# Optimization experiments

Hardware: AMD Instinct MI355X
Metric: run time of the kernel (lower is better)

## Reference

```python
import jax, jax.numpy as jnp
import numpy as np
from jax import lax

PATCH = 9
DILATION = 1
EPS = 1e-6


def _l2norm(x):
    # L2-normalize over channel dim (dim=1), eps added to sum of squares before sqrt
    norm = jnp.sqrt(jnp.sum(x * x, axis=1, keepdims=True) + EPS)
    return x / norm


def setup_inputs() -> dict:
    key = jax.random.key(0)
    k1, k2 = jax.random.split(key)
    feature1 = jax.random.normal(k1, (4, 64, 64, 64), dtype=jnp.float32)
    feature2 = jax.random.normal(k2, (4, 64, 64, 64), dtype=jnp.float32)
    return {"feature1": feature1, "feature2": feature2}


def _correlation(f1, f2, patch, dilation):
    # SpatialCorrelationSampler with ks=1, stride=1, pad=0:
    # corr[b, pi, pj, y, x] = sum_c f1[b,c,y,x] * f2[b,c,y+dy,x+dx]
    # dy = (pi - patch//2)*dilation, dx = (pj - patch//2)*dilation; OOB = 0.
    b, c, h, w = f1.shape
    half = (patch // 2) * dilation
    f2p = jnp.pad(f2, ((0, 0), (0, 0), (half, half), (half, half)))
    d = jnp.arange(patch, dtype=jnp.int32) * dilation  # offsets into padded map
    offs = jnp.stack(jnp.meshgrid(d, d, indexing="ij"), axis=-1).reshape(-1, 2)  # [P^2, 2]

    def one_disp(off):
        f2s = lax.dynamic_slice(f2p, (0, 0, off[0], off[1]), (b, c, h, w))
        return jnp.sum(f1 * f2s, axis=1)  # [b, h, w]

    corr = lax.map(one_disp, offs)  # [P^2, b, h, w] (sequential -> low peak memory)
    return jnp.transpose(corr, (1, 0, 2, 3))  # [b, P^2, h, w]


def reference(feature1, feature2):
    f1 = _l2norm(feature1)
    f2 = _l2norm(feature2)
    b, c, h, w = f1.shape
    corr = _correlation(f1, f2, PATCH, DILATION)  # [b, P^2, h, w]
    corr = corr.reshape(b, PATCH * PATCH, h * w)
    return jax.nn.relu(corr)
```

## Files before the change

kernel.cpp:

```cpp
#include <hip/hip_runtime.h>

#define BB 4
#define CC 64
#define C2 32
#define HH 64
#define WW 64
#define PATCH 9
#define HALF 4
#define P2 81
#define HW (HH * WW)
#define IMG (CC * HW)

typedef _Float16 v2h __attribute__((ext_vector_type(2)));


__global__ __launch_bounds__(128) void prep_kernel(const float* __restrict__ f1,
                                                   const float* __restrict__ f2,
                                                   unsigned* __restrict__ nf) {
    int gid = blockIdx.x * 128 + threadIdx.x;
    int img = gid >> 14;
    int b   = (gid >> 12) & 3;
    int p   = gid & 4095;
    const float* src = (img ? f2 : f1) + b * IMG + p;
    float v[CC];
    float ss = 0.f;
#pragma unroll
    for (int c = 0; c < CC; ++c) { float t = src[c * HW]; v[c] = t; ss += t * t; }
    float inv = rsqrtf(ss + 1e-6f);
    unsigned* dst = nf + img * 524288 + b * 131072 + p;
#pragma unroll
    for (int c2 = 0; c2 < C2; ++c2) {
        v2h h = { (_Float16)(v[2 * c2] * inv), (_Float16)(v[2 * c2 + 1] * inv) };
        dst[c2 * 4096] = __builtin_bit_cast(unsigned, h);
    }
}

__global__ __launch_bounds__(576) void corr_kernel(const unsigned* __restrict__ nf,
                                                   float* __restrict__ out) {
    __shared__ unsigned sB[PATCH * C2 * 72];
    __shared__ unsigned sA[C2 * 64];

    const int tid = threadIdx.x;
    const int x  = tid & 63;
    const int dy = tid >> 6;
    const int b  = blockIdx.x >> 6;
    const int y  = blockIdx.x & 63;

    const unsigned* nf1b = nf + b * 131072;
    const unsigned* nf2b = nf + 524288 + b * 131072;

    if (tid < 512) {
        int c2 = tid >> 4, k = tid & 15;
        *(uint4*)&sA[c2 * 64 + k * 4] = *(const uint4*)&nf1b[c2 * 4096 + y * 64 + k * 4];
    }
#pragma unroll
    for (int it = 0; it < 8; ++it) {
        int item = tid + it * 576;
        int dyy = item >> 9;
        int rem = item & 511;
        int c2 = rem >> 4, k = rem & 15;
        int y2 = y + dyy - HALF;
        uint4 vv = {0u, 0u, 0u, 0u};
        if ((unsigned)y2 < HH)
            vv = *(const uint4*)&nf2b[c2 * 4096 + y2 * 64 + k * 4];
        *(uint4*)&sB[(dyy * C2 + c2) * 72 + 4 + k * 4] = vv;
    }
#pragma unroll
    for (int j = tid; j < 2304; j += 576) {
        int row = j >> 3, e = j & 7;
        sB[row * 72 + (e < 4 ? e : 64 + e)] = 0u;
    }
    __syncthreads();

    float acc[PATCH];
#pragma unroll
    for (int i = 0; i < PATCH; ++i) acc[i] = 0.f;

#pragma unroll
    for (int c2 = 0; c2 < C2; ++c2) {
        v2h a2 = __builtin_bit_cast(v2h, sA[c2 * 64 + x]);
        const unsigned* br = &sB[(dy * C2 + c2) * 72 + x];
#pragma unroll
        for (int dx = 0; dx < PATCH; ++dx)
            acc[dx] = __builtin_amdgcn_fdot2(a2, __builtin_bit_cast(v2h, br[dx]),
                                             acc[dx], false);
    }

    float* ob = out + b * P2 * HW + y * WW + x;
#pragma unroll
    for (int dx = 0; dx < PATCH; ++dx)
        ob[(dy * PATCH + dx) * HW] = fmaxf(acc[dx], 0.f);
}

extern "C" void kernel_launch(void* const* d_in, const int* in_sizes, int n_in,
                              void* d_out, int out_size, void* d_ws, size_t ws_size,
                              hipStream_t stream) {
    const float* f1 = (const float*)d_in[0];
    const float* f2 = (const float*)d_in[1];
    float* out = (float*)d_out;
    unsigned* nf = (unsigned*)d_ws;

    prep_kernel<<<256, 128, 0, stream>>>(f1, f2, nf);
    corr_kernel<<<BB * HH, 576, 0, stream>>>(nf, out);
}
```

Measured before the change: 70.76 us.

## Fuse L2 normalization into correlation kernel via post-scaling by inverse norms

Removes the separate prep kernel that normalized and packed features to fp16 in a workspace. The correlation kernel now reads raw fp32 features, packs them to fp16 in shared memory, computes inverse norms per pixel from the shared tiles, and scales the dot products by both norms before the ReLU. This eliminates one launch and a global-memory round trip. In exchange it reads twice the bytes per staged element, recomputes norms redundantly across blocks, and rounds unnormalized values to fp16.

New measurement: 70.34 us. Within noise of the previous version (-0.6%).

```diff
diff --git a/kernel.cpp b/kernel.cpp
--- a/kernel.cpp
+++ b/kernel.cpp
@@ -8,37 +8,23 @@
 #define PATCH 9
 #define HALF 4
 #define P2 81
-#define HW (HH * WW)
+#define HW 4096
 #define IMG (CC * HW)
 
 typedef _Float16 v2h __attribute__((ext_vector_type(2)));
 
-
-__global__ __launch_bounds__(128) void prep_kernel(const float* __restrict__ f1,
-                                                   const float* __restrict__ f2,
-                                                   unsigned* __restrict__ nf) {
-    int gid = blockIdx.x * 128 + threadIdx.x;
-    int img = gid >> 14;
-    int b   = (gid >> 12) & 3;
-    int p   = gid & 4095;
-    const float* src = (img ? f2 : f1) + b * IMG + p;
-    float v[CC];
-    float ss = 0.f;
-#pragma unroll
-    for (int c = 0; c < CC; ++c) { float t = src[c * HW]; v[c] = t; ss += t * t; }
-    float inv = rsqrtf(ss + 1e-6f);
-    unsigned* dst = nf + img * 524288 + b * 131072 + p;
-#pragma unroll
-    for (int c2 = 0; c2 < C2; ++c2) {
-        v2h h = { (_Float16)(v[2 * c2] * inv), (_Float16)(v[2 * c2 + 1] * inv) };
-        dst[c2 * 4096] = __builtin_bit_cast(unsigned, h);
-    }
+static __device__ __forceinline__ unsigned pk(float a, float b) {
+    v2h h = {(_Float16)a, (_Float16)b};
+    return __builtin_bit_cast(unsigned, h);
 }
 
-__global__ __launch_bounds__(576) void corr_kernel(const unsigned* __restrict__ nf,
+__global__ __launch_bounds__(576) void corr_kernel(const float* __restrict__ f1,
+                                                   const float* __restrict__ f2,
                                                    float* __restrict__ out) {
     __shared__ unsigned sB[PATCH * C2 * 72];
     __shared__ unsigned sA[C2 * 64];
+    __shared__ float sS2[PATCH * 72];
+    __shared__ float sS1[64];
 
     const int tid = threadIdx.x;
     const int x  = tid & 63;
@@ -46,12 +32,15 @@
     const int b  = blockIdx.x >> 6;
     const int y  = blockIdx.x & 63;
 
-    const unsigned* nf1b = nf + b * 131072;
-    const unsigned* nf2b = nf + 524288 + b * 131072;
+    const float* f1r = f1 + b * IMG + y * WW;
+    const float* f2b = f2 + b * IMG;
 
     if (tid < 512) {
         int c2 = tid >> 4, k = tid & 15;
-        *(uint4*)&sA[c2 * 64 + k * 4] = *(const uint4*)&nf1b[c2 * 4096 + y * 64 + k * 4];
+        float4 va = *(const float4*)(f1r + (2 * c2) * HW + 4 * k);
+        float4 vb = *(const float4*)(f1r + (2 * c2 + 1) * HW + 4 * k);
+        uint4 u = {pk(va.x, vb.x), pk(va.y, vb.y), pk(va.z, vb.z), pk(va.w, vb.w)};
+        *(uint4*)&sA[c2 * 64 + 4 * k] = u;
     }
 #pragma unroll
     for (int it = 0; it < 8; ++it) {
@@ -60,10 +49,15 @@
         int rem = item & 511;
         int c2 = rem >> 4, k = rem & 15;
         int y2 = y + dyy - HALF;
-        uint4 vv = {0u, 0u, 0u, 0u};
-        if ((unsigned)y2 < HH)
-            vv = *(const uint4*)&nf2b[c2 * 4096 + y2 * 64 + k * 4];
-        *(uint4*)&sB[(dyy * C2 + c2) * 72 + 4 + k * 4] = vv;
+        uint4 u = {0u, 0u, 0u, 0u};
+        if ((unsigned)y2 < HH) {
+            const float* p = f2b + y2 * WW + 4 * k;
+            float4 va = *(const float4*)(p + (2 * c2) * HW);
+            float4 vb = *(const float4*)(p + (2 * c2 + 1) * HW);
+            u.x = pk(va.x, vb.x); u.y = pk(va.y, vb.y);
+            u.z = pk(va.z, vb.z); u.w = pk(va.w, vb.w);
+        }
+        *(uint4*)&sB[(dyy * C2 + c2) * 72 + 4 + 4 * k] = u;
     }
 #pragma unroll
     for (int j = tid; j < 2304; j += 576) {
@@ -72,10 +66,33 @@
     }
     __syncthreads();
 
+    for (int t = tid; t < 712; t += 576) {
+        float ss = 0.f;
+        if (t < 648) {
+            int row = t / 72, col = t - row * 72;
+            const unsigned* p = &sB[row * C2 * 72 + col];
+#pragma unroll
+            for (int c2 = 0; c2 < C2; ++c2) {
+                v2h v = __builtin_bit_cast(v2h, p[c2 * 72]);
+                ss = __builtin_amdgcn_fdot2(v, v, ss, false);
+            }
+            sS2[t] = rsqrtf(ss + 1e-6f);
+        } else {
+            int col = t - 648;
+            const unsigned* p = &sA[col];
+#pragma unroll
+            for (int c2 = 0; c2 < C2; ++c2) {
+                v2h v = __builtin_bit_cast(v2h, p[c2 * 64]);
+                ss = __builtin_amdgcn_fdot2(v, v, ss, false);
+            }
+            sS1[col] = rsqrtf(ss + 1e-6f);
+        }
+    }
+    __syncthreads();
+
     float acc[PATCH];
 #pragma unroll
     for (int i = 0; i < PATCH; ++i) acc[i] = 0.f;
-
 #pragma unroll
     for (int c2 = 0; c2 < C2; ++c2) {
         v2h a2 = __builtin_bit_cast(v2h, sA[c2 * 64 + x]);
@@ -86,10 +103,11 @@
                                              acc[dx], false);
     }
 
+    const float s1 = sS1[x];
     float* ob = out + b * P2 * HW + y * WW + x;
 #pragma unroll
     for (int dx = 0; dx < PATCH; ++dx)
-        ob[(dy * PATCH + dx) * HW] = fmaxf(acc[dx], 0.f);
+        ob[(dy * PATCH + dx) * HW] = fmaxf(acc[dx] * s1 * sS2[dy * 72 + x + dx], 0.f);
 }
 
 extern "C" void kernel_launch(void* const* d_in, const int* in_sizes, int n_in,
@@ -98,8 +116,7 @@
     const float* f1 = (const float*)d_in[0];
     const float* f2 = (const float*)d_in[1];
     float* out = (float*)d_out;
-    unsigned* nf = (unsigned*)d_ws;
+    (void)d_ws; (void)ws_size;
 
-    prep_kernel<<<256, 128, 0, stream>>>(f1, f2, nf);
-    corr_kernel<<<BB * HH, 576, 0, stream>>>(nf, out);
+    corr_kernel<<<BB * HH, 576, 0, stream>>>(f1, f2, out);
 }
```
